# Optimization experiments

Hardware: AMD Instinct MI355X
Metric: run time of the kernel (lower is better)

The kernel has to match this reference:

```python
import jax, jax.numpy as jnp
import numpy as np

NUM_GRAPHS = 128
NUM_LAYERS = 3
BN_EPS = 1e-5


def setup_inputs() -> dict:
    key = jax.random.key(0)
    ks = jax.random.split(key, 8)
    N, E, D, C = 100000, 1250000, 64, 10
    x = jax.random.normal(ks[0], (N, D), dtype=jnp.float32)
    edge_index = jax.random.randint(ks[1], (2, E), 0, N, dtype=jnp.int64)
    batch = jnp.sort(jax.random.randint(ks[2], (N,), 0, NUM_GRAPHS, dtype=jnp.int64))
    W_rel = jax.random.normal(ks[3], (NUM_LAYERS, D, D), dtype=jnp.float32) * (1.0 / np.sqrt(D))
    b_rel = jax.random.normal(ks[4], (NUM_LAYERS, D), dtype=jnp.float32) * 0.01
    W_root = jax.random.normal(ks[5], (NUM_LAYERS, D, D), dtype=jnp.float32) * (1.0 / np.sqrt(D))
    gamma = jnp.ones((NUM_LAYERS, D), dtype=jnp.float32)
    beta = jnp.zeros((NUM_LAYERS, D), dtype=jnp.float32)
    W_cls = jax.random.normal(ks[6], (D, C), dtype=jnp.float32) * (1.0 / np.sqrt(D))
    b_cls = jnp.zeros((C,), dtype=jnp.float32)
    return {"x": x, "edge_index": edge_index, "batch": batch,
            "W_rel": W_rel, "b_rel": b_rel, "W_root": W_root,
            "gamma": gamma, "beta": beta, "W_cls": W_cls, "b_cls": b_cls}


def reference(x, edge_index, batch, W_rel, b_rel, W_root, gamma, beta, W_cls, b_cls):
    N = x.shape[0]
    src, dst = edge_index[0], edge_index[1]
    for l in range(NUM_LAYERS):
        # GraphConv: lin_rel(sum-aggregated neighbor feats) + lin_root(x)
        msg = jax.ops.segment_sum(x[src], dst, num_segments=N)  # [N, D]
        h = msg @ W_rel[l] + b_rel[l] + x @ W_root[l]
        # BatchNorm1d over nodes (batch statistics, training-mode math)
        mean = jnp.mean(h, axis=0)
        var = jnp.var(h, axis=0)
        h = (h - mean) * jax.lax.rsqrt(var + BN_EPS) * gamma[l] + beta[l]
        x = jax.nn.relu(h)  # dropout is identity at inference
    # global_mean_pool: segment mean over graph ids
    counts = jax.ops.segment_sum(jnp.ones((N,), dtype=x.dtype), batch, num_segments=NUM_GRAPHS)
    pooled = jax.ops.segment_sum(x, batch, num_segments=NUM_GRAPHS)
    pooled = pooled / jnp.maximum(counts, 1.0)[:, None]  # [G, D]
    return pooled @ W_cls + b_cls
```

## Files before the change

kernel.cpp:

```cpp
#include <hip/hip_runtime.h>

#define D 64
#define NGRAPH 128
#define NCLS 10
#define BN_EPS 1e-5f
#define BUCK_SZ 512
#define EPB 8192

typedef __attribute__((ext_vector_type(8))) __bf16 bf16x8;
typedef __attribute__((ext_vector_type(4))) float floatx4;

union BF8 { bf16x8 v; ushort u[8]; };

__device__ __forceinline__ unsigned f2bf_rne(float f) {
  unsigned u = __float_as_uint(f);
  return (u + 0x7FFFu + ((u >> 16) & 1u)) >> 16;
}
__device__ __forceinline__ unsigned pack2bf(float a, float b) {
  return f2bf_rne(a) | (f2bf_rne(b) << 16);
}
__device__ __forceinline__ float4 bf4_to_f4(uint2 u) {
  float4 r;
  r.x = __uint_as_float(u.x << 16);
  r.y = __uint_as_float(u.x & 0xFFFF0000u);
  r.z = __uint_as_float(u.y << 16);
  r.w = __uint_as_float(u.y & 0xFFFF0000u);
  return r;
}

__device__ __forceinline__ void split8(float4 a, float4 b,
                                       bf16x8* hi, bf16x8* lo) {
  float f[8] = {a.x, a.y, a.z, a.w, b.x, b.y, b.z, b.w};
  BF8 H, L;
#pragma unroll
  for (int t = 0; t < 8; t++) {
    unsigned u = __float_as_uint(f[t]);
    H.u[t] = (ushort)(u >> 16);
    float hf = __uint_as_float(u & 0xFFFF0000u);
    float lf = f[t] - hf;
    L.u[t] = (ushort)(__float_as_uint(lf) >> 16);
  }
  *hi = H.v;
  *lo = L.v;
}

__global__ __launch_bounds__(256) void bucket_scatter_kernel(
    const int* __restrict__ ei, int* __restrict__ gcnt, int* __restrict__ pk,
    int E, int capB, int nbuck) {
  __shared__ int hist[256];
  __shared__ int base[256];
  int t = threadIdx.x;
  int e0 = blockIdx.x * EPB;
  int e1 = min(e0 + EPB, E);
  hist[t] = 0;
  __syncthreads();
  for (int e = e0 + t; e < e1; e += 256)
    atomicAdd(&hist[ei[E + e] >> 9], 1);
  __syncthreads();
  int h = hist[t];
  if (t < nbuck && h > 0) base[t] = atomicAdd(&gcnt[t], h);
  hist[t] = 0;
  __syncthreads();
  for (int e = e0 + t; e < e1; e += 256) {
    int s = ei[e];
    int d = ei[E + e];
    int b = d >> 9;
    int pos = base[b] + atomicAdd(&hist[b], 1);
    if (pos < capB) pk[(size_t)b * capB + pos] = (s << 9) | (d & (BUCK_SZ - 1));
  }
}

__global__ void bucket_scan_kernel(const int* __restrict__ gcnt,
                                   int* __restrict__ bstart,
                                   int* __restrict__ row_start,
                                   int nbuck, int N, int capB) {
  __shared__ int s[256];
  int t = threadIdx.x;
  int v = (t < nbuck) ? min(gcnt[t], capB) : 0;
  s[t] = v;
  __syncthreads();
  for (int off = 1; off < 256; off <<= 1) {
    int add = (t >= off) ? s[t - off] : 0;
    __syncthreads();
    s[t] += add;
    __syncthreads();
  }
  if (t < nbuck) bstart[t] = s[t] - v;
  if (t == 0) {
    bstart[nbuck] = s[255];
    row_start[N] = s[255];
  }
}

__global__ __launch_bounds__(256) void bucket_place_kernel(
    const int* __restrict__ pk, const int* __restrict__ gcnt,
    const int* __restrict__ bstart, int* __restrict__ row_start,
    int* __restrict__ csr_src, int N, int capB) {
  __shared__ int hist[BUCK_SZ];
  __shared__ int scn[256];
  __shared__ int cur[BUCK_SZ];
  int b = blockIdx.x;
  int t = threadIdx.x;
  hist[t] = 0;
  hist[t + 256] = 0;
  int cnt = min(gcnt[b], capB);
  const int* seg = pk + (size_t)b * capB;
  __syncthreads();
  for (int e = t; e < cnt; e += 256)
    atomicAdd(&hist[seg[e] & (BUCK_SZ - 1)], 1);
  __syncthreads();
  scn[t] = hist[2 * t] + hist[2 * t + 1];
  __syncthreads();
  for (int off = 1; off < 256; off <<= 1) {
    int add = (t >= off) ? scn[t - off] : 0;
    __syncthreads();
    scn[t] += add;
    __syncthreads();
  }
  int base = bstart[b];
  int ex = (t == 0) ? 0 : scn[t - 1];
  int c0 = base + ex;
  int c1 = c0 + hist[2 * t];
  cur[2 * t] = c0;
  cur[2 * t + 1] = c1;
  int dst0 = b * BUCK_SZ + 2 * t;
  if (dst0 < N) row_start[dst0] = c0;
  if (dst0 + 1 < N) row_start[dst0 + 1] = c1;
  __syncthreads();
  for (int e = t; e < cnt; e += 256) {
    int p = seg[e];
    int slot = atomicAdd(&cur[p & (BUCK_SZ - 1)], 1);
    csr_src[slot] = p >> 9;
  }
}

__global__ __launch_bounds__(256) void wsplit_kernel(
    const float* __restrict__ Wrel, const float* __restrict__ Wroot,
    ushort* __restrict__ wfrag) {
  int l = blockIdx.x;
  const float* Wr = Wrel + l * 4096;
  const float* Wo = Wroot + l * 4096;
  ushort* base = wfrag + l * 16384;
  for (int slot = threadIdx.x; slot < 1024; slot += 256) {
    int kt = slot >> 8, nt = (slot >> 6) & 3, lane = slot & 63;
    int quad = lane >> 4, c = lane & 15;
    ushort* ph = base + (((kt * 4 + nt) * 2 + 0) * 64 + lane) * 8;
    ushort* pl = base + (((kt * 4 + nt) * 2 + 1) * 64 + lane) * 8;
#pragma unroll
    for (int j = 0; j < 8; j++) {
      int k = kt * 32 + quad * 8 + j;
      int n = nt * 16 + c;
      float w = (k < 64) ? Wr[k * 64 + n] : Wo[(k - 64) * 64 + n];
      unsigned u = __float_as_uint(w);
      ph[j] = (ushort)(u >> 16);
      float lf = w - __uint_as_float(u & 0xFFFF0000u);
      pl[j] = (ushort)(__float_as_uint(lf) >> 16);
    }
  }
}

__global__ __launch_bounds__(256) void xprep_kernel(
    const float* __restrict__ x, ushort* __restrict__ xbf, int n) {
  int base = (blockIdx.x * 256 + threadIdx.x) * 8;
  if (base >= n) return;
  float4 a = *(const float4*)(x + base);
  float4 b = *(const float4*)(x + base + 4);
  uint4 o;
  o.x = pack2bf(a.x, a.y);
  o.y = pack2bf(a.z, a.w);
  o.z = pack2bf(b.x, b.y);
  o.w = pack2bf(b.z, b.w);
  *(uint4*)(xbf + base) = o;
}

__global__ __launch_bounds__(256) void gather_kernel(
    const ushort* __restrict__ xbf, const int* __restrict__ csr_src,
    const int* __restrict__ row_start, const float* __restrict__ scsh,
    int apply, float* __restrict__ msg, int N) {
  int i = blockIdx.x * 4 + (threadIdx.x >> 6);
  int lane = threadIdx.x & 63;
  int q = lane >> 4;
  int f = (lane & 15) << 2;
  if (i >= N) return;
  int e0 = row_start[i], e1 = row_start[i + 1];
  int cnt = e1 - e0;
  int myidx = csr_src[e0 + lane];
  float4 acc = {0.f, 0.f, 0.f, 0.f};
  float4 sc, sh;
  if (apply) {
    sc = *(const float4*)&scsh[f];
    sh = *(const float4*)&scsh[D + f];
  }

  int cnt64 = min(cnt, 64);
  for (int base = 0; base < cnt64; base += 16) {
    int j0 = base + q;
    int s0 = __shfl(myidx, j0);
    int s1 = __shfl(myidx, j0 + 4);
    int s2 = __shfl(myidx, j0 + 8);
    int s3 = __shfl(myidx, j0 + 12);
    float m0 = (j0 < cnt) ? 1.f : 0.f;
    float m1 = (j0 + 4 < cnt) ? 1.f : 0.f;
    float m2 = (j0 + 8 < cnt) ? 1.f : 0.f;
    float m3 = (j0 + 12 < cnt) ? 1.f : 0.f;
    s0 = (j0 < cnt) ? s0 : 0;
    s1 = (j0 + 4 < cnt) ? s1 : 0;
    s2 = (j0 + 8 < cnt) ? s2 : 0;
    s3 = (j0 + 12 < cnt) ? s3 : 0;
    float4 v0 = bf4_to_f4(*(const uint2*)(xbf + (size_t)s0 * D + f));
    float4 v1 = bf4_to_f4(*(const uint2*)(xbf + (size_t)s1 * D + f));
    float4 v2 = bf4_to_f4(*(const uint2*)(xbf + (size_t)s2 * D + f));
    float4 v3 = bf4_to_f4(*(const uint2*)(xbf + (size_t)s3 * D + f));
    if (apply) {
      acc.x += m0 * fmaxf(v0.x * sc.x + sh.x, 0.f) + m1 * fmaxf(v1.x * sc.x + sh.x, 0.f)
             + m2 * fmaxf(v2.x * sc.x + sh.x, 0.f) + m3 * fmaxf(v3.x * sc.x + sh.x, 0.f);
      acc.y += m0 * fmaxf(v0.y * sc.y + sh.y, 0.f) + m1 * fmaxf(v1.y * sc.y + sh.y, 0.f)
             + m2 * fmaxf(v2.y * sc.y + sh.y, 0.f) + m3 * fmaxf(v3.y * sc.y + sh.y, 0.f);
      acc.z += m0 * fmaxf(v0.z * sc.z + sh.z, 0.f) + m1 * fmaxf(v1.z * sc.z + sh.z, 0.f)
             + m2 * fmaxf(v2.z * sc.z + sh.z, 0.f) + m3 * fmaxf(v3.z * sc.z + sh.z, 0.f);
      acc.w += m0 * fmaxf(v0.w * sc.w + sh.w, 0.f) + m1 * fmaxf(v1.w * sc.w + sh.w, 0.f)
             + m2 * fmaxf(v2.w * sc.w + sh.w, 0.f) + m3 * fmaxf(v3.w * sc.w + sh.w, 0.f);
    } else {
      acc.x += m0 * v0.x + m1 * v1.x + m2 * v2.x + m3 * v3.x;
      acc.y += m0 * v0.y + m1 * v1.y + m2 * v2.y + m3 * v3.y;
      acc.z += m0 * v0.z + m1 * v1.z + m2 * v2.z + m3 * v3.z;
      acc.w += m0 * v0.w + m1 * v1.w + m2 * v2.w + m3 * v3.w;
    }
  }

  for (int e = e0 + 64 + q; e < e1; e += 4) {
    float4 v = bf4_to_f4(*(const uint2*)(xbf + (size_t)csr_src[e] * D + f));
    if (apply) {
      acc.x += fmaxf(v.x * sc.x + sh.x, 0.f);
      acc.y += fmaxf(v.y * sc.y + sh.y, 0.f);
      acc.z += fmaxf(v.z * sc.z + sh.z, 0.f);
      acc.w += fmaxf(v.w * sc.w + sh.w, 0.f);
    } else {
      acc.x += v.x; acc.y += v.y; acc.z += v.z; acc.w += v.w;
    }
  }

  acc.x += __shfl_xor(acc.x, 16); acc.x += __shfl_xor(acc.x, 32);
  acc.y += __shfl_xor(acc.y, 16); acc.y += __shfl_xor(acc.y, 32);
  acc.z += __shfl_xor(acc.z, 16); acc.z += __shfl_xor(acc.z, 32);
  acc.w += __shfl_xor(acc.w, 16); acc.w += __shfl_xor(acc.w, 32);
  if (q == 0) *(float4*)(msg + (size_t)i * D + f) = acc;
}

__global__ __launch_bounds__(256, 1) void mm_mfma_kernel(
    const float* msg, const float* xf32, const ushort* xbfin,
    const ushort* __restrict__ wfrag, const float* __restrict__ brel,
    const float* __restrict__ scsh, int apply,
    float* h, ushort* hbf, int wh, int wbf, float* __restrict__ stats,
    int N, int ntiles, int nwaves) {
  __shared__ float ssum[4][64];
  __shared__ float ssq[4][64];
  int tid = threadIdx.x;
  int lane = tid & 63;
  int wvid = tid >> 6;
  int wv = (blockIdx.x * 256 + tid) >> 6;
  int quad = lane >> 4;
  int lo4 = lane & 15;

  bf16x8 bf[4][4][2];
#pragma unroll
  for (int kt = 0; kt < 4; kt++)
#pragma unroll
    for (int nt = 0; nt < 4; nt++)
#pragma unroll
      for (int s = 0; s < 2; s++)
        bf[kt][nt][s] =
            *(const bf16x8*)(wfrag + (((kt * 4 + nt) * 2 + s) * 64 + lane) * 8);

  float bias[4];
#pragma unroll
  for (int nt = 0; nt < 4; nt++) bias[nt] = brel[nt * 16 + lo4];

  float scx[2][8], shx[2][8];
  if (apply) {
#pragma unroll
    for (int hh = 0; hh < 2; hh++)
#pragma unroll
      for (int jj = 0; jj < 8; jj++) {
        int f = hh * 32 + quad * 8 + jj;
        scx[hh][jj] = scsh[f];
        shx[hh][jj] = scsh[D + f];
      }
  }

  float psum[4] = {0.f, 0.f, 0.f, 0.f};
  float psq[4] = {0.f, 0.f, 0.f, 0.f};

  for (int t = wv; t < ntiles; t += nwaves) {
    int i0 = t * 16;
    int row = i0 + lo4;
    if (row >= N) row = N - 1;
    bf16x8 ahi[4], alo[4];
#pragma unroll
    for (int kt = 0; kt < 4; kt++) {
      float4 a, b;
      if (kt < 2) {
        const float* p = msg + (size_t)row * D + (kt & 1) * 32 + quad * 8;
        a = *(const float4*)p;
        b = *(const float4*)(p + 4);
      } else if (apply) {
        const ushort* p = xbfin + (size_t)row * D + (kt & 1) * 32 + quad * 8;
        uint4 u = *(const uint4*)p;
        uint2 ulo = {u.x, u.y}, uhi = {u.z, u.w};
        a = bf4_to_f4(ulo);
        b = bf4_to_f4(uhi);
        int hh = kt - 2;
        a.x = fmaxf(a.x * scx[hh][0] + shx[hh][0], 0.f);
        a.y = fmaxf(a.y * scx[hh][1] + shx[hh][1], 0.f);
        a.z = fmaxf(a.z * scx[hh][2] + shx[hh][2], 0.f);
        a.w = fmaxf(a.w * scx[hh][3] + shx[hh][3], 0.f);
        b.x = fmaxf(b.x * scx[hh][4] + shx[hh][4], 0.f);
        b.y = fmaxf(b.y * scx[hh][5] + shx[hh][5], 0.f);
        b.z = fmaxf(b.z * scx[hh][6] + shx[hh][6], 0.f);
        b.w = fmaxf(b.w * scx[hh][7] + shx[hh][7], 0.f);
      } else {
        const float* p = xf32 + (size_t)row * D + (kt & 1) * 32 + quad * 8;
        a = *(const float4*)p;
        b = *(const float4*)(p + 4);
      }
      split8(a, b, &ahi[kt], &alo[kt]);
    }
#pragma unroll
    for (int nt = 0; nt < 4; nt++) {
      floatx4 acc = {bias[nt], bias[nt], bias[nt], bias[nt]};
#pragma unroll
      for (int kt = 0; kt < 4; kt++) {
        acc = __builtin_amdgcn_mfma_f32_16x16x32_bf16(ahi[kt], bf[kt][nt][0],
                                                      acc, 0, 0, 0);
        acc = __builtin_amdgcn_mfma_f32_16x16x32_bf16(ahi[kt], bf[kt][nt][1],
                                                      acc, 0, 0, 0);
        acc = __builtin_amdgcn_mfma_f32_16x16x32_bf16(alo[kt], bf[kt][nt][0],
                                                      acc, 0, 0, 0);
      }
#pragma unroll
      for (int r = 0; r < 4; r++) {
        int grow = i0 + quad * 4 + r;
        if (grow < N) {
          float v = acc[r];
          size_t idx = (size_t)grow * D + nt * 16 + lo4;
          if (wh) h[idx] = v;
          if (wbf) hbf[idx] = (ushort)f2bf_rne(v);
          psum[nt] += v;
          psq[nt] += v * v;
        }
      }
    }
  }

#pragma unroll
  for (int nt = 0; nt < 4; nt++) {
    float s = psum[nt], q = psq[nt];
    s += __shfl_xor(s, 16); s += __shfl_xor(s, 32);
    q += __shfl_xor(q, 16); q += __shfl_xor(q, 32);
    if (lane < 16) { ssum[wvid][nt * 16 + lane] = s; ssq[wvid][nt * 16 + lane] = q; }
  }
  __syncthreads();
  if (tid < 64) {
    atomicAdd(&stats[tid], ssum[0][tid] + ssum[1][tid] + ssum[2][tid] + ssum[3][tid]);
  } else if (tid < 128) {
    int c = tid - 64;
    atomicAdd(&stats[D + c], ssq[0][c] + ssq[1][c] + ssq[2][c] + ssq[3][c]);
  }
}

__global__ void bn_finalize_kernel(float* __restrict__ stats,
                                   const float* __restrict__ gamma,
                                   const float* __restrict__ beta,
                                   float* __restrict__ scsh, float fN) {
  int j = threadIdx.x;
  float mean = stats[j] / fN;
  float var = stats[D + j] / fN - mean * mean;
  float sc = gamma[j] * rsqrtf(var + BN_EPS);
  scsh[j] = sc;
  scsh[D + j] = beta[j] - mean * sc;
  stats[j] = 0.f;
  stats[D + j] = 0.f;
}

__global__ __launch_bounds__(256) void norm_relu_pool_kernel(
    const float* __restrict__ h, const float* __restrict__ scsh,
    const int* __restrict__ batch, float* __restrict__ pooled, int N) {
  int j = threadIdx.x & 63;
  int q = threadIdx.x >> 6;
  int i0 = blockIdx.x * 256;
  float sc = scsh[j], sh = scsh[D + j];
  int curg = -1;
  float acc = 0.f;
  for (int r = q; r < 256; r += 4) {
    int i = i0 + r;
    if (i >= N) break;
    int b = batch[i];
    float v = fmaxf(h[(size_t)i * D + j] * sc + sh, 0.f);
    if (b != curg) {
      if (curg >= 0) atomicAdd(&pooled[curg * D + j], acc);
      curg = b;
      acc = v;
    } else {
      acc += v;
    }
  }
  if (curg >= 0) atomicAdd(&pooled[curg * D + j], acc);
}

__global__ void counts_kernel(const int* __restrict__ batch,
                              float* __restrict__ counts, int N) {
  int g = threadIdx.x;
  if (g >= NGRAPH) return;
  int lo = 0, hi = N;
  while (lo < hi) { int m = (lo + hi) >> 1; if (batch[m] < g) lo = m + 1; else hi = m; }
  int start = lo;
  lo = 0; hi = N;
  while (lo < hi) { int m = (lo + hi) >> 1; if (batch[m] <= g) lo = m + 1; else hi = m; }
  counts[g] = (float)(lo - start);
}

__global__ void cls_kernel(const float* __restrict__ pooled,
                           const float* __restrict__ counts,
                           const float* __restrict__ Wcls,
                           const float* __restrict__ bcls,
                           float* __restrict__ out) {
  int tid = blockIdx.x * blockDim.x + threadIdx.x;
  if (tid >= NGRAPH * NCLS) return;
  int g = tid / NCLS, c = tid % NCLS;
  float inv = 1.f / fmaxf(counts[g], 1.f);
  float acc = bcls[c];
#pragma unroll 8
  for (int k = 0; k < D; k++) acc += pooled[g * D + k] * inv * Wcls[k * NCLS + c];
  out[g * NCLS + c] = acc;
}

extern "C" void kernel_launch(void* const* d_in, const int* in_sizes, int n_in,
                              void* d_out, int out_size, void* d_ws, size_t ws_size,
                              hipStream_t stream) {
  const float* x      = (const float*)d_in[0];
  const int*   ei     = (const int*)d_in[1];
  const int*   batch  = (const int*)d_in[2];
  const float* W_rel  = (const float*)d_in[3];
  const float* b_rel  = (const float*)d_in[4];
  const float* W_root = (const float*)d_in[5];
  const float* gamma  = (const float*)d_in[6];
  const float* beta   = (const float*)d_in[7];
  const float* W_cls  = (const float*)d_in[8];
  const float* b_cls  = (const float*)d_in[9];
  float* out = (float*)d_out;

  int E = in_sizes[1] / 2;
  int N = in_sizes[2];
  size_t nd = (size_t)N * D;
  int nbuck = (N + BUCK_SZ - 1) / BUCK_SZ;
  int capB = ((2 * E / nbuck) + 511) & ~511;
  if (capB < 1024) capB = 1024;

  float* bufA    = (float*)d_ws;
  float* bufB    = bufA + nd;
  ushort* xbf    = (ushort*)(bufB + nd);
  float* stats   = (float*)(xbf + nd);
  float* scsh    = stats + 2 * D;
  float* pooled  = scsh + 2 * D;
  float* counts  = pooled + NGRAPH * D;
  int* gcnt      = (int*)(counts + NGRAPH);
  ushort* wfrag  = (ushort*)(gcnt + ((nbuck + 3) & ~3));
  int* bstart    = (int*)(wfrag + 3 * 16384);
  int* row_start = bstart + nbuck + 1;
  int* csr_src   = row_start + N + 1;
  int* pk        = csr_src + E;

  size_t zero_bytes = (size_t)(2 * D + 2 * D + NGRAPH * D + NGRAPH) * 4 +
                      (size_t)nbuck * 4;
  hipMemsetAsync(stats, 0, zero_bytes, stream);

  bucket_scatter_kernel<<<(E + EPB - 1) / EPB, 256, 0, stream>>>(
      ei, gcnt, pk, E, capB, nbuck);
  bucket_scan_kernel<<<1, 256, 0, stream>>>(gcnt, bstart, row_start, nbuck, N, capB);
  bucket_place_kernel<<<nbuck, 256, 0, stream>>>(pk, gcnt, bstart, row_start,
                                                 csr_src, N, capB);
  wsplit_kernel<<<3, 256, 0, stream>>>(W_rel, W_root, wfrag);
  xprep_kernel<<<(int)((nd / 8 + 255) / 256), 256, 0, stream>>>(x, xbf, (int)nd);

  const int MM_BLOCKS = 512;
  const int MM_WAVES = MM_BLOCKS * 4;
  int ntiles = (N + 15) / 16;
  for (int l = 0; l < 3; l++) {
    int apply = (l > 0) ? 1 : 0;
    int wbf = (l < 2) ? 1 : 0;
    int wh = (l == 2) ? 1 : 0;

    gather_kernel<<<(N + 3) / 4, 256, 0, stream>>>(xbf, csr_src, row_start,
                                                   scsh, apply, bufB, N);

    mm_mfma_kernel<<<MM_BLOCKS, 256, 0, stream>>>(
        bufB, x, xbf, wfrag + l * 16384, b_rel + l * D, scsh, apply,
        bufA, xbf , wh, wbf, stats,
        N, ntiles, MM_WAVES);

    bn_finalize_kernel<<<1, 64, 0, stream>>>(stats, gamma + l * D, beta + l * D,
                                             scsh, (float)N);
  }

  norm_relu_pool_kernel<<<(N + 255) / 256, 256, 0, stream>>>(bufA, scsh, batch,
                                                             pooled, N);
  counts_kernel<<<1, 128, 0, stream>>>(batch, counts, N);
  cls_kernel<<<(NGRAPH * NCLS + 255) / 256, 256, 0, stream>>>(pooled, counts,
                                                              W_cls, b_cls, out);
}
```

Baseline: 357.9 us.

## Fold BN finalize and counts kernels into consumers; widen gather loads to 16 bytes

```diff
diff --git a/kernel.cpp b/kernel.cpp
--- a/kernel.cpp
+++ b/kernel.cpp
@@ -26,6 +26,16 @@
   r.z = __uint_as_float(u.y << 16);
   r.w = __uint_as_float(u.y & 0xFFFF0000u);
   return r;
+}
+
+__device__ __forceinline__ void bn_sc_sh(
+    const float* __restrict__ stats, const float* __restrict__ gamma,
+    const float* __restrict__ beta, float fN, int f, float* sc, float* sh) {
+  float mean = stats[f] / fN;
+  float var = stats[D + f] / fN - mean * mean;
+  float s = gamma[f] * rsqrtf(var + BN_EPS);
+  *sc = s;
+  *sh = beta[f] - mean * s;
 }
 
 __device__ __forceinline__ void split8(float4 a, float4 b,
@@ -175,83 +185,90 @@
 
 __global__ __launch_bounds__(256) void gather_kernel(
     const ushort* __restrict__ xbf, const int* __restrict__ csr_src,
-    const int* __restrict__ row_start, const float* __restrict__ scsh,
-    int apply, float* __restrict__ msg, int N) {
+    const int* __restrict__ row_start, const float* __restrict__ stats_prev,
+    const float* __restrict__ gamma, const float* __restrict__ beta,
+    float fN, int apply, float* __restrict__ msg, int N) {
   int i = blockIdx.x * 4 + (threadIdx.x >> 6);
   int lane = threadIdx.x & 63;
-  int q = lane >> 4;
-  int f = (lane & 15) << 2;
+  int es = lane >> 3;
+  int f = (lane & 7) << 3;
   if (i >= N) return;
   int e0 = row_start[i], e1 = row_start[i + 1];
   int cnt = e1 - e0;
   int myidx = csr_src[e0 + lane];
-  float4 acc = {0.f, 0.f, 0.f, 0.f};
-  float4 sc, sh;
+
+  float sc[8], sh[8];
   if (apply) {
-    sc = *(const float4*)&scsh[f];
-    sh = *(const float4*)&scsh[D + f];
-  }
-
+#pragma unroll
+    for (int k = 0; k < 8; k++)
+      bn_sc_sh(stats_prev, gamma, beta, fN, f + k, &sc[k], &sh[k]);
+  }
+
+  float acc[8] = {0.f, 0.f, 0.f, 0.f, 0.f, 0.f, 0.f, 0.f};
   int cnt64 = min(cnt, 64);
   for (int base = 0; base < cnt64; base += 16) {
-    int j0 = base + q;
+    int j0 = base + es;
+    int j1 = base + 8 + es;
     int s0 = __shfl(myidx, j0);
-    int s1 = __shfl(myidx, j0 + 4);
-    int s2 = __shfl(myidx, j0 + 8);
-    int s3 = __shfl(myidx, j0 + 12);
+    int s1 = __shfl(myidx, j1);
     float m0 = (j0 < cnt) ? 1.f : 0.f;
-    float m1 = (j0 + 4 < cnt) ? 1.f : 0.f;
-    float m2 = (j0 + 8 < cnt) ? 1.f : 0.f;
-    float m3 = (j0 + 12 < cnt) ? 1.f : 0.f;
+    float m1 = (j1 < cnt) ? 1.f : 0.f;
     s0 = (j0 < cnt) ? s0 : 0;
-    s1 = (j0 + 4 < cnt) ? s1 : 0;
-    s2 = (j0 + 8 < cnt) ? s2 : 0;
-    s3 = (j0 + 12 < cnt) ? s3 : 0;
-    float4 v0 = bf4_to_f4(*(const uint2*)(xbf + (size_t)s0 * D + f));
-    float4 v1 = bf4_to_f4(*(const uint2*)(xbf + (size_t)s1 * D + f));
-    float4 v2 = bf4_to_f4(*(const uint2*)(xbf + (size_t)s2 * D + f));
-    float4 v3 = bf4_to_f4(*(const uint2*)(xbf + (size_t)s3 * D + f));
+    s1 = (j1 < cnt) ? s1 : 0;
+    uint4 u0 = *(const uint4*)(xbf + (size_t)s0 * D + f);
+    uint4 u1 = *(const uint4*)(xbf + (size_t)s1 * D + f);
+    uint2 a0 = {u0.x, u0.y}, b0 = {u0.z, u0.w};
+    uint2 a1 = {u1.x, u1.y}, b1 = {u1.z, u1.w};
+    float4 v0l = bf4_to_f4(a0), v0h = bf4_to_f4(b0);
+    float4 v1l = bf4_to_f4(a1), v1h = bf4_to_f4(b1);
+    float w0[8] = {v0l.x, v0l.y, v0l.z, v0l.w, v0h.x, v0h.y, v0h.z, v0h.w};
+    float w1[8] = {v1l.x, v1l.y, v1l.z, v1l.w, v1h.x, v1h.y, v1h.z, v1h.w};
     if (apply) {
-      acc.x += m0 * fmaxf(v0.x * sc.x + sh.x, 0.f) + m1 * fmaxf(v1.x * sc.x + sh.x, 0.f)
-             + m2 * fmaxf(v2.x * sc.x + sh.x, 0.f) + m3 * fmaxf(v3.x * sc.x + sh.x, 0.f);
-      acc.y += m0 * fmaxf(v0.y * sc.y + sh.y, 0.f) + m1 * fmaxf(v1.y * sc.y + sh.y, 0.f)
-             + m2 * fmaxf(v2.y * sc.y + sh.y, 0.f) + m3 * fmaxf(v3.y * sc.y + sh.y, 0.f);
-      acc.z += m0 * fmaxf(v0.z * sc.z + sh.z, 0.f) + m1 * fmaxf(v1.z * sc.z + sh.z, 0.f)
-             + m2 * fmaxf(v2.z * sc.z + sh.z, 0.f) + m3 * fmaxf(v3.z * sc.z + sh.z, 0.f);
-      acc.w += m0 * fmaxf(v0.w * sc.w + sh.w, 0.f) + m1 * fmaxf(v1.w * sc.w + sh.w, 0.f)
-             + m2 * fmaxf(v2.w * sc.w + sh.w, 0.f) + m3 * fmaxf(v3.w * sc.w + sh.w, 0.f);
+#pragma unroll
+      for (int k = 0; k < 8; k++)
+        acc[k] += m0 * fmaxf(w0[k] * sc[k] + sh[k], 0.f)
+                + m1 * fmaxf(w1[k] * sc[k] + sh[k], 0.f);
     } else {
-      acc.x += m0 * v0.x + m1 * v1.x + m2 * v2.x + m3 * v3.x;
-      acc.y += m0 * v0.y + m1 * v1.y + m2 * v2.y + m3 * v3.y;
-      acc.z += m0 * v0.z + m1 * v1.z + m2 * v2.z + m3 * v3.z;
-      acc.w += m0 * v0.w + m1 * v1.w + m2 * v2.w + m3 * v3.w;
+#pragma unroll
+      for (int k = 0; k < 8; k++)
+        acc[k] += m0 * w0[k] + m1 * w1[k];
     }
   }
 
-  for (int e = e0 + 64 + q; e < e1; e += 4) {
-    float4 v = bf4_to_f4(*(const uint2*)(xbf + (size_t)csr_src[e] * D + f));
+  for (int e = e0 + 64 + es; e < e1; e += 8) {
+    uint4 u = *(const uint4*)(xbf + (size_t)csr_src[e] * D + f);
+    uint2 a = {u.x, u.y}, b = {u.z, u.w};
+    float4 vl = bf4_to_f4(a), vh = bf4_to_f4(b);
+    float w[8] = {vl.x, vl.y, vl.z, vl.w, vh.x, vh.y, vh.z, vh.w};
     if (apply) {
-      acc.x += fmaxf(v.x * sc.x + sh.x, 0.f);
-      acc.y += fmaxf(v.y * sc.y + sh.y, 0.f);
-      acc.z += fmaxf(v.z * sc.z + sh.z, 0.f);
-      acc.w += fmaxf(v.w * sc.w + sh.w, 0.f);
+#pragma unroll
+      for (int k = 0; k < 8; k++) acc[k] += fmaxf(w[k] * sc[k] + sh[k], 0.f);
     } else {
-      acc.x += v.x; acc.y += v.y; acc.z += v.z; acc.w += v.w;
+#pragma unroll
+      for (int k = 0; k < 8; k++) acc[k] += w[k];
     }
   }
 
-  acc.x += __shfl_xor(acc.x, 16); acc.x += __shfl_xor(acc.x, 32);
-  acc.y += __shfl_xor(acc.y, 16); acc.y += __shfl_xor(acc.y, 32);
-  acc.z += __shfl_xor(acc.z, 16); acc.z += __shfl_xor(acc.z, 32);
-  acc.w += __shfl_xor(acc.w, 16); acc.w += __shfl_xor(acc.w, 32);
-  if (q == 0) *(float4*)(msg + (size_t)i * D + f) = acc;
+#pragma unroll
+  for (int k = 0; k < 8; k++) {
+    acc[k] += __shfl_xor(acc[k], 8);
+    acc[k] += __shfl_xor(acc[k], 16);
+    acc[k] += __shfl_xor(acc[k], 32);
+  }
+  if (es == 0) {
+    float4 lo = {acc[0], acc[1], acc[2], acc[3]};
+    float4 hi = {acc[4], acc[5], acc[6], acc[7]};
+    *(float4*)(msg + (size_t)i * D + f) = lo;
+    *(float4*)(msg + (size_t)i * D + f + 4) = hi;
+  }
 }
 
 __global__ __launch_bounds__(256, 1) void mm_mfma_kernel(
     const float* msg, const float* xf32, const ushort* xbfin,
     const ushort* __restrict__ wfrag, const float* __restrict__ brel,
-    const float* __restrict__ scsh, int apply,
-    float* h, ushort* hbf, int wh, int wbf, float* __restrict__ stats,
+    const float* __restrict__ stats_prev, const float* __restrict__ gamma,
+    const float* __restrict__ beta, float fN, int apply,
+    float* h, ushort* hbf, int wh, int wbf, float* __restrict__ stats_cur,
     int N, int ntiles, int nwaves) {
   __shared__ float ssum[4][64];
   __shared__ float ssq[4][64];
@@ -283,8 +300,7 @@
 #pragma unroll
       for (int jj = 0; jj < 8; jj++) {
         int f = hh * 32 + quad * 8 + jj;
-        scx[hh][jj] = scsh[f];
-        shx[hh][jj] = scsh[D + f];
+        bn_sc_sh(stats_prev, gamma, beta, fN, f, &scx[hh][jj], &shx[hh][jj]);
       }
   }
 
@@ -361,34 +377,25 @@
   }
   __syncthreads();
   if (tid < 64) {
-    atomicAdd(&stats[tid], ssum[0][tid] + ssum[1][tid] + ssum[2][tid] + ssum[3][tid]);
+    atomicAdd(&stats_cur[tid],
+              ssum[0][tid] + ssum[1][tid] + ssum[2][tid] + ssum[3][tid]);
   } else if (tid < 128) {
     int c = tid - 64;
-    atomicAdd(&stats[D + c], ssq[0][c] + ssq[1][c] + ssq[2][c] + ssq[3][c]);
-  }
-}
-
-__global__ void bn_finalize_kernel(float* __restrict__ stats,
-                                   const float* __restrict__ gamma,
-                                   const float* __restrict__ beta,
-                                   float* __restrict__ scsh, float fN) {
-  int j = threadIdx.x;
-  float mean = stats[j] / fN;
-  float var = stats[D + j] / fN - mean * mean;
-  float sc = gamma[j] * rsqrtf(var + BN_EPS);
-  scsh[j] = sc;
-  scsh[D + j] = beta[j] - mean * sc;
-  stats[j] = 0.f;
-  stats[D + j] = 0.f;
+    atomicAdd(&stats_cur[D + c],
+              ssq[0][c] + ssq[1][c] + ssq[2][c] + ssq[3][c]);
+  }
 }
 
 __global__ __launch_bounds__(256) void norm_relu_pool_kernel(
-    const float* __restrict__ h, const float* __restrict__ scsh,
-    const int* __restrict__ batch, float* __restrict__ pooled, int N) {
+    const float* __restrict__ h, const float* __restrict__ stats,
+    const float* __restrict__ gamma, const float* __restrict__ beta,
+    float fN, const int* __restrict__ batch, float* __restrict__ pooled,
+    int N) {
   int j = threadIdx.x & 63;
   int q = threadIdx.x >> 6;
   int i0 = blockIdx.x * 256;
-  float sc = scsh[j], sh = scsh[D + j];
+  float sc, sh;
+  bn_sc_sh(stats, gamma, beta, fN, j, &sc, &sh);
   int curg = -1;
   float acc = 0.f;
   for (int r = q; r < 256; r += 4) {
@@ -407,27 +414,20 @@
   if (curg >= 0) atomicAdd(&pooled[curg * D + j], acc);
 }
 
-__global__ void counts_kernel(const int* __restrict__ batch,
-                              float* __restrict__ counts, int N) {
-  int g = threadIdx.x;
-  if (g >= NGRAPH) return;
+__global__ void cls_kernel(const float* __restrict__ pooled,
+                           const int* __restrict__ batch,
+                           const float* __restrict__ Wcls,
+                           const float* __restrict__ bcls,
+                           float* __restrict__ out, int N) {
+  int tid = blockIdx.x * blockDim.x + threadIdx.x;
+  if (tid >= NGRAPH * NCLS) return;
+  int g = tid / NCLS, c = tid % NCLS;
   int lo = 0, hi = N;
   while (lo < hi) { int m = (lo + hi) >> 1; if (batch[m] < g) lo = m + 1; else hi = m; }
   int start = lo;
   lo = 0; hi = N;
   while (lo < hi) { int m = (lo + hi) >> 1; if (batch[m] <= g) lo = m + 1; else hi = m; }
-  counts[g] = (float)(lo - start);
-}
-
-__global__ void cls_kernel(const float* __restrict__ pooled,
-                           const float* __restrict__ counts,
-                           const float* __restrict__ Wcls,
-                           const float* __restrict__ bcls,
-                           float* __restrict__ out) {
-  int tid = blockIdx.x * blockDim.x + threadIdx.x;
-  if (tid >= NGRAPH * NCLS) return;
-  int g = tid / NCLS, c = tid % NCLS;
-  float inv = 1.f / fmaxf(counts[g], 1.f);
+  float inv = 1.f / fmaxf((float)(lo - start), 1.f);
   float acc = bcls[c];
 #pragma unroll 8
   for (int k = 0; k < D; k++) acc += pooled[g * D + k] * inv * Wcls[k * NCLS + c];
@@ -455,24 +455,23 @@
   int nbuck = (N + BUCK_SZ - 1) / BUCK_SZ;
   int capB = ((2 * E / nbuck) + 511) & ~511;
   if (capB < 1024) capB = 1024;
+  float fN = (float)N;
 
   float* bufA    = (float*)d_ws;
   float* bufB    = bufA + nd;
   ushort* xbf    = (ushort*)(bufB + nd);
-  float* stats   = (float*)(xbf + nd);
-  float* scsh    = stats + 2 * D;
-  float* pooled  = scsh + 2 * D;
-  float* counts  = pooled + NGRAPH * D;
-  int* gcnt      = (int*)(counts + NGRAPH);
+  float* stats3  = (float*)(xbf + nd);
+  float* pooled  = stats3 + 3 * 2 * D;
+  int* gcnt      = (int*)(pooled + NGRAPH * D);
   ushort* wfrag  = (ushort*)(gcnt + ((nbuck + 3) & ~3));
   int* bstart    = (int*)(wfrag + 3 * 16384);
   int* row_start = bstart + nbuck + 1;
   int* csr_src   = row_start + N + 1;
   int* pk        = csr_src + E;
 
-  size_t zero_bytes = (size_t)(2 * D + 2 * D + NGRAPH * D + NGRAPH) * 4 +
+  size_t zero_bytes = (size_t)(3 * 2 * D + NGRAPH * D) * 4 +
                       (size_t)nbuck * 4;
-  hipMemsetAsync(stats, 0, zero_bytes, stream);
+  hipMemsetAsync(stats3, 0, zero_bytes, stream);
 
   bucket_scatter_kernel<<<(E + EPB - 1) / EPB, 256, 0, stream>>>(
       ei, gcnt, pk, E, capB, nbuck);
@@ -489,22 +488,25 @@
     int apply = (l > 0) ? 1 : 0;
     int wbf = (l < 2) ? 1 : 0;
     int wh = (l == 2) ? 1 : 0;
-
-    gather_kernel<<<(N + 3) / 4, 256, 0, stream>>>(xbf, csr_src, row_start,
-                                                   scsh, apply, bufB, N);
+    const float* st_prev = stats3 + (l > 0 ? (l - 1) * 2 * D : 0);
+    const float* gm_prev = gamma + (l > 0 ? (l - 1) * D : 0);
+    const float* bt_prev = beta + (l > 0 ? (l - 1) * D : 0);
+    float* st_cur = stats3 + l * 2 * D;
+
+    gather_kernel<<<(N + 3) / 4, 256, 0, stream>>>(
+        xbf, csr_src, row_start, st_prev, gm_prev, bt_prev, fN, apply,
+        bufB, N);
 
     mm_mfma_kernel<<<MM_BLOCKS, 256, 0, stream>>>(
-        bufB, x, xbf, wfrag + l * 16384, b_rel + l * D, scsh, apply,
-        bufA, xbf , wh, wbf, stats,
+        bufB, x, xbf, wfrag + l * 16384, b_rel + l * D,
+        st_prev, gm_prev, bt_prev, fN, apply,
+        bufA, xbf , wh, wbf, st_cur,
         N, ntiles, MM_WAVES);
-
-    bn_finalize_kernel<<<1, 64, 0, stream>>>(stats, gamma + l * D, beta + l * D,
-                                             scsh, (float)N);
-  }
-
-  norm_relu_pool_kernel<<<(N + 255) / 256, 256, 0, stream>>>(bufA, scsh, batch,
-                                                             pooled, N);
-  counts_kernel<<<1, 128, 0, stream>>>(batch, counts, N);
-  cls_kernel<<<(NGRAPH * NCLS + 255) / 256, 256, 0, stream>>>(pooled, counts,
-                                                              W_cls, b_cls, out);
-}
+  }
+
+  norm_relu_pool_kernel<<<(N + 255) / 256, 256, 0, stream>>>(
+      bufA, stats3 + 2 * 2 * D, gamma + 2 * D, beta + 2 * D, fN, batch,
+      pooled, N);
+  cls_kernel<<<(NGRAPH * NCLS + 255) / 256, 256, 0, stream>>>(
+      pooled, batch, W_cls, b_cls, out, N);
+}
```

New measurement: 426.6 us. 19.2% more time.
